# Performance work log

Hardware: AMD Instinct MI355X
Metric: run time of the kernel (lower is better)

The kernel has to match this reference:

```python
import jax, jax.numpy as jnp
import numpy as np

EMB, HEADS, T_BLK = 1024, 16, 2048
B, T = 2, 2048
HD = EMB // HEADS


def setup_inputs() -> dict:
    key = jax.random.key(0)
    ks = jax.random.split(key, 9)
    s = 1.0 / np.sqrt(EMB)
    return {
        "x": jax.random.normal(ks[0], (B, T, EMB), jnp.float32),
        "Wq": jax.random.normal(ks[1], (EMB, EMB), jnp.float32) * s,
        "bq": jax.random.normal(ks[2], (EMB,), jnp.float32) * s,
        "Wk": jax.random.normal(ks[3], (EMB, EMB), jnp.float32) * s,
        "bk": jax.random.normal(ks[4], (EMB,), jnp.float32) * s,
        "Wv": jax.random.normal(ks[5], (EMB, EMB), jnp.float32) * s,
        "bv": jax.random.normal(ks[6], (EMB,), jnp.float32) * s,
        "Wo": jax.random.normal(ks[7], (EMB, EMB), jnp.float32) * s,
        "bo": jax.random.normal(ks[8], (EMB,), jnp.float32) * s,
    }


def reference(x, Wq, bq, Wk, bk, Wv, bv, Wo, bo):
    # eval mode: dropout is identity
    Bn, Tn, C = x.shape
    def proj(W, b):
        y = x @ W.T + b                      # [B,T,C]
        return y.reshape(Bn, Tn, HEADS, HD).transpose(0, 2, 1, 3)  # [B,H,T,hd]
    q, k, v = proj(Wq, bq), proj(Wk, bk), proj(Wv, bv)
    scores = jnp.einsum('bhqd,bhkd->bhqk', q, k) * (HD ** -0.5)  # [B,H,T,T]
    causal = jnp.tril(jnp.ones((Tn, Tn), dtype=bool))
    scores = jnp.where(causal, scores, -jnp.inf)
    w = jax.nn.softmax(scores, axis=-1)
    out = jnp.einsum('bhqk,bhkd->bhqd', w, v)                    # [B,H,T,hd]
    out = out.transpose(0, 2, 1, 3).reshape(Bn, Tn, C)
    return out @ Wo.T + bo
```

## Files before the change

kernel.cpp:

```cpp
#include <hip/hip_runtime.h>
#include <stdint.h>

#define EMB   1024
#define HEADS 16
#define HD    64
#define BB    2
#define TT    2048
#define MTOT  (BB*TT)

#define ELX (4194304u)
#define ELW (1048576u)

#define CSCALE (0.125f * 1.44269504088896f)

typedef __attribute__((ext_vector_type(8))) short short8;
typedef __attribute__((ext_vector_type(4))) float f32x4;
typedef __attribute__((ext_vector_type(4))) unsigned short us4;

__device__ __forceinline__ float bf2f(ushort u) {
  union { uint32_t u; float f; } x; x.u = ((uint32_t)u) << 16; return x.f;
}
__device__ __forceinline__ ushort f2bf(float f) {
  union { float f; uint32_t u; } x; x.f = f;
  uint32_t u = x.u;
  u += 0x7fffu + ((u >> 16) & 1u);
  return (ushort)(u >> 16);
}
__device__ __forceinline__ uint32_t pack2(uint32_t lo, uint32_t hi) {
  return (lo >> 16) | (hi & 0xFFFF0000u);
}
__device__ __forceinline__ short8 pack8(f32x4 a, f32x4 b) {
  union { f32x4 v; uint32_t u[4]; } A, B;
  A.v = a; B.v = b;
  union { uint32_t d[4]; short8 s; } R;
  R.d[0] = pack2(A.u[0], A.u[1]);
  R.d[1] = pack2(A.u[2], A.u[3]);
  R.d[2] = pack2(B.u[0], B.u[1]);
  R.d[3] = pack2(B.u[2], B.u[3]);
  return R.s;
}
__device__ __forceinline__ short8 cvt8_rne(const float* f) {
  f32x4 a = *(const f32x4*)f;
  f32x4 b = *(const f32x4*)(f + 4);
  short8 r;
  r[0] = (short)f2bf(a[0]); r[1] = (short)f2bf(a[1]);
  r[2] = (short)f2bf(a[2]); r[3] = (short)f2bf(a[3]);
  r[4] = (short)f2bf(b[0]); r[5] = (short)f2bf(b[1]);
  r[6] = (short)f2bf(b[2]); r[7] = (short)f2bf(b[3]);
  return r;
}

__device__ __forceinline__ void gll16(const void* g, void* l) {
  __builtin_amdgcn_global_load_lds((const __attribute__((address_space(1))) void*)g,
                                   (__attribute__((address_space(3))) void*)l,
                                   16, 0, 0);
}

__device__ __forceinline__ int probe_dtype(const uint32_t* __restrict__ x) {
  const int lane = threadIdx.x & 63;
  int cnt = 0;
#pragma unroll
  for (int i = 0; i < 4; ++i) {
    const uint32_t v = x[lane * 4 + i];
    const uint32_t e = ((v & 0xFFFFu) >> 7) & 0xFFu;
    cnt += (e >= 0x70u && e <= 0x8Fu) ? 1 : 0;
  }
#pragma unroll
  for (int off = 1; off < 64; off <<= 1) cnt += __shfl_xor(cnt, off);
  return (cnt > 128) ? 1 : 0;
}

__global__ __launch_bounds__(256) void convert4(const void* __restrict__ w0,
                                                const void* __restrict__ w1,
                                                const void* __restrict__ w2,
                                                const void* __restrict__ x,
                                                ushort* __restrict__ w3,
                                                ushort* __restrict__ xb,
                                                int* __restrict__ flag) {
  const int isbf = probe_dtype((const uint32_t*)x);
  if (blockIdx.x == 0 && threadIdx.x == 0) *flag = isbf;
  const size_t i = ((size_t)blockIdx.x * 256 + threadIdx.x) * 8;
  if (i < 3u * ELW) {
    const int wi = (int)(i >> 20);
    const size_t off = i & (ELW - 1);
    const void* src = (wi == 0) ? w0 : (wi == 1) ? w1 : w2;
    if (isbf) *(short8*)(w3 + i) = *(const short8*)((const ushort*)src + off);
    else      *(short8*)(w3 + i) = cvt8_rne((const float*)src + off);
  } else {
    const size_t j = i - 3u * ELW;
    if (isbf) *(short8*)(xb + j) = *(const short8*)((const ushort*)x + j);
    else      *(short8*)(xb + j) = cvt8_rne((const float*)x + j);
  }
}

#define ASZ (256 * 64)
#define BSZ (192 * 64)

__device__ __forceinline__ void qkv_core(const ushort* __restrict__ xb,
                                         const ushort* __restrict__ W,
                                         int m0, int n0r,
                                         ushort* As0, ushort* Bs0,
                                         f32x4 acc[8][3]) {
  const int tid  = threadIdx.x;
  const int w    = tid >> 6;
  const int lane = tid & 63;
  const int quad = lane >> 4;
  const int l16  = lane & 15;
  const int wr   = w >> 2, wc = w & 3;

  const int prow = tid >> 3;
  const int c    = tid & 7;
  const int sw   = c ^ (prow & 7);
  const int rsw  = l16 & 7;

  auto stageB = [&](ushort* dst, int kt) {
#pragma unroll
    for (int g = 0; g < 3; ++g)
      gll16(W + (size_t)(n0r + g * 64 + prow) * EMB + kt * 64 + sw * 8,
            dst + g * 4096 + w * 512);
  };
  auto stageA = [&](ushort* dst, int kt) {
#pragma unroll
    for (int g = 0; g < 4; ++g)
      gll16(xb + (size_t)(m0 + g * 64 + prow) * EMB + kt * 64 + sw * 8,
            dst + g * 4096 + w * 512);
  };
  auto compute = [&](const ushort* Ab, const ushort* Bb) {
    short8 bf_[3][2];
#pragma unroll
    for (int ni = 0; ni < 3; ++ni)
#pragma unroll
      for (int ks = 0; ks < 2; ++ks)
        bf_[ni][ks] = *(const short8*)&Bb[(wc * 48 + ni * 16 + l16) * 64 +
                                          ((ks * 4 + quad) ^ rsw) * 8];
#pragma unroll
    for (int mi = 0; mi < 8; ++mi) {
      const int arow = (wr * 128 + mi * 16 + l16) * 64;
      short8 a0 = *(const short8*)&Ab[arow + ((quad) ^ rsw) * 8];
      short8 a1 = *(const short8*)&Ab[arow + ((4 + quad) ^ rsw) * 8];
#pragma unroll
      for (int ni = 0; ni < 3; ++ni) {
        acc[mi][ni] = __builtin_amdgcn_mfma_f32_16x16x32_bf16(a0, bf_[ni][0], acc[mi][ni], 0, 0, 0);
        acc[mi][ni] = __builtin_amdgcn_mfma_f32_16x16x32_bf16(a1, bf_[ni][1], acc[mi][ni], 0, 0, 0);
      }
    }
  };

  stageB(Bs0, 0);
  stageA(As0, 0);
  __syncthreads();

  for (int tp = 0; tp < 8; ++tp) {
    const int t0 = 2 * tp;
    stageB(Bs0 + BSZ, t0 + 1);
    stageA(As0 + ASZ, t0 + 1);
    compute(As0, Bs0);
    __syncthreads();
    if (tp < 7) {
      stageB(Bs0, t0 + 2);
      stageA(As0, t0 + 2);
    }
    compute(As0 + ASZ, Bs0 + BSZ);
    __syncthreads();
  }
}

__global__ __launch_bounds__(512, 2) void qkv_pipe(const ushort* __restrict__ xb,
                                                   const ushort* __restrict__ w3,
                                                   const void* __restrict__ bq,
                                                   const void* __restrict__ bk,
                                                   const void* __restrict__ bv,
                                                   ushort* __restrict__ qo,
                                                   ushort* __restrict__ ko,
                                                   ushort* __restrict__ vo,
                                                   const int* __restrict__ flag) {
  __shared__ __align__(16) ushort As2[2 * ASZ];
  __shared__ __align__(16) ushort Bs2[2 * BSZ];
  const int bid = blockIdx.x;
  const int xcd = bid & 7;
  const int mt  = xcd * 2 + ((bid >> 3) & 1);
  const int nt  = bid >> 4;
  const int m0  = mt * 256;
  const int n0r = nt * 192;

  f32x4 acc[8][3];
#pragma unroll
  for (int a = 0; a < 8; ++a)
#pragma unroll
    for (int b = 0; b < 3; ++b) acc[a][b] = (f32x4){0.f, 0.f, 0.f, 0.f};

  qkv_core(xb, w3, m0, n0r, As2, Bs2, acc);

  const int isbf = *flag;
  const int tid  = threadIdx.x;
  const int w    = tid >> 6;
  const int lane = tid & 63;
  const int quad = lane >> 4;
  const int l16  = lane & 15;
  const int wr   = w >> 2, wc = w & 3;

#pragma unroll
  for (int ni = 0; ni < 3; ++ni) {
    const int n   = n0r + wc * 48 + ni * 16 + l16;
    const int mat = n >> 10, nn = n & 1023;
    const void* bias = (mat == 0) ? bq : (mat == 1) ? bk : bv;
    const float bv_ = isbf ? bf2f(((const ushort*)bias)[nn]) : ((const float*)bias)[nn];
    const int h = nn >> 6, d = nn & 63;
    const float sc = (mat == 0) ? CSCALE : 1.0f;
    ushort* dqk = (mat == 0) ? qo : ko;
#pragma unroll
    for (int mi = 0; mi < 8; ++mi) {
      const int m = m0 + wr * 128 + mi * 16 + quad * 4;
      const int b = m >> 11, tt = m & (TT - 1);
      if (mat == 2) {
        us4 pk;
#pragma unroll
        for (int r = 0; r < 4; ++r) pk[r] = f2bf(acc[mi][ni][r] + bv_);
        *(us4*)&vo[((size_t)((b * HEADS + h) * HD + d)) * TT + tt] = pk;
      } else {
#pragma unroll
        for (int r = 0; r < 4; ++r)
          dqk[((size_t)((b * HEADS + h) * TT + tt + r)) * HD + d] =
              f2bf((acc[mi][ni][r] + bv_) * sc);
      }
    }
  }
}

__global__ __launch_bounds__(256) void attn3(const ushort* __restrict__ qw,
                                             const ushort* __restrict__ kw,
                                             const ushort* __restrict__ vtw,
                                             ushort* __restrict__ out) {
  __shared__ __align__(16) ushort Ks[2][64 * 64];
  __shared__ __align__(16) ushort Vts[2][64 * 64];
  __shared__ __align__(16) ushort Ps[4][16 * 64];

  const int bid = blockIdx.x;
  const int j  = bid >> 8;
  const int r8 = bid & 255;
  const int qh = r8 & 31;
  const int bh = j * 8 + (r8 >> 5);
  int qt;
  if      (j == 0) qt = qh;
  else if (j == 1) qt = 31 - qh;
  else if (j == 2) qt = (qh + 16) & 31;
  else             qt = 31 - ((qh + 16) & 31);
  const int h = bh & (HEADS - 1);
  const int b = bh >> 4;

  const int tid  = threadIdx.x;
  const int w    = tid >> 6;
  const int lane = tid & 63;
  const int quad = lane >> 4;
  const int l16  = lane & 15;
  const int rsw  = l16 & 7;

  const size_t hoff = ((size_t)(b * HEADS + h)) * TT * HD;
  const ushort* Qg = qw + hoff;
  const ushort* Kg = kw + hoff;
  const ushort* Vg = vtw + hoff;
  const int q0 = qt * 64;

  short8 qf[2];
  {
    const ushort* qrow = Qg + (size_t)(q0 + w * 16 + l16) * HD;
    qf[0] = *(const short8*)(qrow + quad * 8);
    qf[1] = *(const short8*)(qrow + 32 + quad * 8);
  }

  const int row = tid >> 2;
  const int cq  = (tid & 3) * 2;
  const int s0  = (cq)     ^ (row & 7);
  const int s1  = (cq + 1) ^ (row & 7);
  const int c0  = cq * 8;
  const ushort* Kbase = Kg + (size_t)row * HD + c0;
  const ushort* Vbase = Vg + (size_t)row * TT + c0;

  float lsp[4] = {0.f, 0.f, 0.f, 0.f};
  f32x4 O[4];
#pragma unroll
  for (int ni = 0; ni < 4; ++ni) O[ni] = (f32x4){0.f, 0.f, 0.f, 0.f};

  auto loadT = [&](int kt, short8& k0, short8& k1, short8& v0, short8& v1) {
    const size_t ko_ = (size_t)kt * 64 * HD;
    k0 = *(const short8*)(Kbase + ko_);
    k1 = *(const short8*)(Kbase + ko_ + 8);
    v0 = *(const short8*)(Vbase + kt * 64);
    v1 = *(const short8*)(Vbase + kt * 64 + 8);
  };
  auto writeT = [&](int buf, short8 k0, short8 k1, short8 v0, short8 v1) {
    *(short8*)&Ks[buf][row * 64 + s0 * 8]  = k0;
    *(short8*)&Ks[buf][row * 64 + s1 * 8]  = k1;
    *(short8*)&Vts[buf][row * 64 + s0 * 8] = v0;
    *(short8*)&Vts[buf][row * 64 + s1 * 8] = v1;
  };

  auto compute_tile = [&](int kt, int buf) {
    f32x4 s[4];
#pragma unroll
    for (int ni = 0; ni < 4; ++ni) s[ni] = (f32x4){0.f, 0.f, 0.f, 0.f};
#pragma unroll
    for (int ks = 0; ks < 2; ++ks) {
#pragma unroll
      for (int ni = 0; ni < 4; ++ni) {
        short8 kb = *(const short8*)&Ks[buf][(ni * 16 + l16) * 64 +
                                            ((ks * 4 + quad) ^ rsw) * 8];
        s[ni] = __builtin_amdgcn_mfma_f32_16x16x32_bf16(kb, qf[ks], s[ni], 0, 0, 0);
      }
    }
    if (kt == qt) {
      const int qq = w * 16 + l16;
#pragma unroll
      for (int ni = 0; ni < 4; ++ni) {
#pragma unroll
        for (int r = 0; r < 4; ++r)
          if (ni * 16 + quad * 4 + r > qq) s[ni][r] = -__builtin_inff();
      }
    }
#pragma unroll
    for (int ni = 0; ni < 4; ++ni) {
      union { float f; uint32_t u; } p0, p1, p2, p3;
      p0.f = exp2f(s[ni][0]); p1.f = exp2f(s[ni][1]);
      p2.f = exp2f(s[ni][2]); p3.f = exp2f(s[ni][3]);
      lsp[ni] += (p0.f + p1.f) + (p2.f + p3.f);
      uint2 dw;
      dw.x = pack2(p0.u, p1.u);
      dw.y = pack2(p2.u, p3.u);
      const int slot = (2 * ni + (quad >> 1)) ^ rsw;
      *(uint2*)&Ps[w][l16 * 64 + slot * 8 + (quad & 1) * 4] = dw;
    }
#pragma unroll
    for (int ks = 0; ks < 2; ++ks) {
      short8 a = *(const short8*)&Ps[w][l16 * 64 + ((ks * 4 + quad) ^ rsw) * 8];
#pragma unroll
      for (int ni = 0; ni < 4; ++ni) {
        short8 vb = *(const short8*)&Vts[buf][(ni * 16 + l16) * 64 +
                                              ((ks * 4 + quad) ^ rsw) * 8];
        O[ni] = __builtin_amdgcn_mfma_f32_16x16x32_bf16(a, vb, O[ni], 0, 0, 0);
      }
    }
  };

  short8 ek0, ek1, ev0, ev1;
  short8 ok0, ok1, ov0, ov1;
  loadT(0, ek0, ek1, ev0, ev1);
  if (qt >= 1) loadT(1, ok0, ok1, ov0, ov1);

  for (int pt = 0; ; ++pt) {
    const int t0 = 2 * pt, t1 = t0 + 1;
    __syncthreads();
    writeT(0, ek0, ek1, ev0, ev1);
    if (t1 <= qt) writeT(1, ok0, ok1, ov0, ov1);
    if (t0 + 2 <= qt) loadT(t0 + 2, ek0, ek1, ev0, ev1);
    if (t1 + 2 <= qt) loadT(t1 + 2, ok0, ok1, ov0, ov1);
    __syncthreads();
    compute_tile(t0, 0);
    if (t1 <= qt) compute_tile(t1, 1);
    if (t1 >= qt) break;
  }

  float lst = (lsp[0] + lsp[1]) + (lsp[2] + lsp[3]);
  lst += __shfl_xor(lst, 16);
  lst += __shfl_xor(lst, 32);

#pragma unroll
  for (int r = 0; r < 4; ++r) {
    const float inv = 1.0f / __shfl(lst, (lane & 48) | (quad * 4 + r));
    const int t = q0 + w * 16 + quad * 4 + r;
#pragma unroll
    for (int ni = 0; ni < 4; ++ni) {
      out[((size_t)(b * TT + t)) * EMB + h * HD + ni * 16 + l16] = f2bf(O[ni][r] * inv);
    }
  }
}

#define PASZ (128 * 64)

template<bool WBF>
__device__ __forceinline__ void proj_core(const ushort* __restrict__ A,
                                          const void* __restrict__ Wo,
                                          int m0, int n0,
                                          ushort* As2, ushort* Bs2,
                                          f32x4 acc[4][2]) {
  const int tid  = threadIdx.x;
  const int w    = tid >> 6;
  const int lane = tid & 63;
  const int quad = lane >> 4;
  const int l16  = lane & 15;
  const int wr   = w >> 2, wc = w & 3;

  const int prow = tid >> 3;
  const int sw   = (tid & 7) ^ (prow & 7);
  const int rsw  = l16 & 7;

  const ushort* Wu = (const ushort*)Wo;
  const float*  Wf = (const float*)Wo;
  f32x4 wreg[4];

  auto stageA = [&](ushort* dst, int kt) {
#pragma unroll
    for (int g = 0; g < 2; ++g)
      gll16(A + (size_t)(m0 + g * 64 + prow) * EMB + kt * 64 + sw * 8,
            dst + g * 4096 + w * 512);
  };
  auto stageB_gll = [&](ushort* dst, int kt) {
#pragma unroll
    for (int g = 0; g < 2; ++g)
      gll16(Wu + (size_t)(n0 + g * 64 + prow) * EMB + kt * 64 + sw * 8,
            dst + g * 4096 + w * 512);
  };
  auto stageB_issue = [&](int kt) {
#pragma unroll
    for (int g = 0; g < 2; ++g) {
      const float* src = Wf + (size_t)(n0 + g * 64 + prow) * EMB + kt * 64 + sw * 8;
      wreg[2 * g]     = *(const f32x4*)(src);
      wreg[2 * g + 1] = *(const f32x4*)(src + 4);
    }
  };
  auto stageB_write = [&](ushort* dst) {
#pragma unroll
    for (int g = 0; g < 2; ++g)
      *(short8*)&dst[((size_t)g * 512 + tid) * 8] = pack8(wreg[2 * g], wreg[2 * g + 1]);
  };
  auto compute = [&](const ushort* Ab, const ushort* Bb) {
    short8 bf_[2][2];
#pragma unroll
    for (int ni = 0; ni < 2; ++ni)
#pragma unroll
      for (int ks = 0; ks < 2; ++ks)
        bf_[ni][ks] = *(const short8*)&Bb[(wc * 32 + ni * 16 + l16) * 64 +
                                          ((ks * 4 + quad) ^ rsw) * 8];
#pragma unroll
    for (int mi = 0; mi < 4; ++mi) {
      const int arow = (wr * 64 + mi * 16 + l16) * 64;
      short8 a0 = *(const short8*)&Ab[arow + ((quad) ^ rsw) * 8];
      short8 a1 = *(const short8*)&Ab[arow + ((4 + quad) ^ rsw) * 8];
#pragma unroll
      for (int ni = 0; ni < 2; ++ni) {
        acc[mi][ni] = __builtin_amdgcn_mfma_f32_16x16x32_bf16(a0, bf_[ni][0], acc[mi][ni], 0, 0, 0);
        acc[mi][ni] = __builtin_amdgcn_mfma_f32_16x16x32_bf16(a1, bf_[ni][1], acc[mi][ni], 0, 0, 0);
      }
    }
  };

  stageA(As2, 0);
  if constexpr (WBF) stageB_gll(Bs2, 0);
  else { stageB_issue(0); stageB_write(Bs2); }
  __syncthreads();

  for (int tp = 0; tp < 8; ++tp) {
    const int t0 = 2 * tp;
    stageA(As2 + PASZ, t0 + 1);
    if constexpr (WBF) stageB_gll(Bs2 + PASZ, t0 + 1);
    else stageB_issue(t0 + 1);
    compute(As2, Bs2);
    if constexpr (!WBF) stageB_write(Bs2 + PASZ);
    __syncthreads();
    if (tp < 7) {
      stageA(As2, t0 + 2);
      if constexpr (WBF) stageB_gll(Bs2, t0 + 2);
      else stageB_issue(t0 + 2);
    }
    compute(As2 + PASZ, Bs2 + PASZ);
    if constexpr (!WBF) { if (tp < 7) stageB_write(Bs2); }
    __syncthreads();
  }
}

__global__ __launch_bounds__(512, 2) void proj_pipe(const ushort* __restrict__ A,
                                                    const void* __restrict__ Wo,
                                                    const void* __restrict__ bo,
                                                    void* __restrict__ out,
                                                    const int* __restrict__ flag) {
  __shared__ __align__(16) ushort As2[2 * PASZ];
  __shared__ __align__(16) ushort Bs2[2 * PASZ];
  const int bid = blockIdx.x;
  const int xcd = bid & 7;
  const int mt  = xcd * 4 + ((bid >> 3) & 3);
  const int nt  = bid >> 5;
  const int m0  = mt * 128;
  const int n0  = nt * 128;

  f32x4 acc[4][2];
#pragma unroll
  for (int i = 0; i < 4; ++i)
#pragma unroll
    for (int jj = 0; jj < 2; ++jj) acc[i][jj] = (f32x4){0.f, 0.f, 0.f, 0.f};

  const int isbf = *flag;
  if (isbf) proj_core<true >(A, Wo, m0, n0, As2, Bs2, acc);
  else      proj_core<false>(A, Wo, m0, n0, As2, Bs2, acc);

  const int tid  = threadIdx.x;
  const int w    = tid >> 6;
  const int lane = tid & 63;
  const int quad = lane >> 4;
  const int l16  = lane & 15;
  const int wr   = w >> 2, wc = w & 3;

#pragma unroll
  for (int ni = 0; ni < 2; ++ni) {
    const int n = n0 + wc * 32 + ni * 16 + l16;
    const float bv_ = isbf ? bf2f(((const ushort*)bo)[n]) : ((const float*)bo)[n];
#pragma unroll
    for (int mi = 0; mi < 4; ++mi) {
#pragma unroll
      for (int r = 0; r < 4; ++r) {
        const int m = m0 + wr * 64 + mi * 16 + quad * 4 + r;
        const float v = acc[mi][ni][r] + bv_;
        if (isbf) ((ushort*)out)[(size_t)m * EMB + n] = f2bf(v);
        else      ((float*) out)[(size_t)m * EMB + n] = v;
      }
    }
  }
}

extern "C" void kernel_launch(void* const* d_in, const int* in_sizes, int n_in,
                              void* d_out, int out_size, void* d_ws, size_t ws_size,
                              hipStream_t stream) {
  const void* x  = d_in[0];
  const void* Wq = d_in[1];
  const void* bq = d_in[2];
  const void* Wk = d_in[3];
  const void* bk = d_in[4];
  const void* Wv = d_in[5];
  const void* bv = d_in[6];
  const void* Wo = d_in[7];
  const void* bo = d_in[8];

  int* flag = (int*)d_ws;
  ushort* base = (ushort*)((char*)d_ws + 256);

  ushort* q_ws  = base;
  ushort* k_ws  = q_ws + ELX;
  ushort* vt_ws = k_ws + ELX;
  ushort* w3    = vt_ws + ELX;
  ushort* o_ws  = vt_ws + ELX;
  ushort* xb    = (ushort*)d_out;

  convert4<<<dim3(3584), dim3(256), 0, stream>>>(Wq, Wk, Wv, x, w3, xb, flag);
  qkv_pipe<<<dim3(256), dim3(512), 0, stream>>>(xb, w3, bq, bk, bv,
                                                q_ws, k_ws, vt_ws, flag);
  attn3<<<dim3(1024), dim3(256), 0, stream>>>(q_ws, k_ws, vt_ws, o_ws);
  proj_pipe<<<dim3(256), dim3(512), 0, stream>>>(o_ws, Wo, bo, d_out, flag);
}
```

Baseline: 199.5 us.

## Retile QKV GEMM to 128x128 single-buffered tiles with more blocks

Replaces the 256x192 double-buffered QKV projection tile (512 threads, 256 blocks) with a 128x128 single-buffered tile on 256 threads and 768 blocks. Each block now covers a single Q/K/V matrix, so the bias pointer and scale are chosen once per block. The aim is better occupancy and load balance across the CUs with less LDS per block. The cost is lower data reuse per tile and no overlap of global loads with MFMA work, since there is now a sync before and after every k-step.

```diff
diff --git a/kernel.cpp b/kernel.cpp
--- a/kernel.cpp
+++ b/kernel.cpp
@@ -93,79 +93,56 @@
   }
 }
 
-#define ASZ (256 * 64)
-#define BSZ (192 * 64)
+#define QSZ (128 * 64)
 
 __device__ __forceinline__ void qkv_core(const ushort* __restrict__ xb,
                                          const ushort* __restrict__ W,
                                          int m0, int n0r,
-                                         ushort* As0, ushort* Bs0,
-                                         f32x4 acc[8][3]) {
+                                         ushort* As, ushort* Bs,
+                                         f32x4 acc[4][4]) {
   const int tid  = threadIdx.x;
   const int w    = tid >> 6;
   const int lane = tid & 63;
   const int quad = lane >> 4;
   const int l16  = lane & 15;
-  const int wr   = w >> 2, wc = w & 3;
+  const int wr   = w >> 1, wc = w & 1;
 
   const int prow = tid >> 3;
-  const int c    = tid & 7;
-  const int sw   = c ^ (prow & 7);
+  const int sw   = (tid & 7) ^ (prow & 7);
   const int rsw  = l16 & 7;
 
-  auto stageB = [&](ushort* dst, int kt) {
-#pragma unroll
-    for (int g = 0; g < 3; ++g)
-      gll16(W + (size_t)(n0r + g * 64 + prow) * EMB + kt * 64 + sw * 8,
-            dst + g * 4096 + w * 512);
-  };
-  auto stageA = [&](ushort* dst, int kt) {
+  for (int kt = 0; kt < 16; ++kt) {
+    __syncthreads();
 #pragma unroll
     for (int g = 0; g < 4; ++g)
-      gll16(xb + (size_t)(m0 + g * 64 + prow) * EMB + kt * 64 + sw * 8,
-            dst + g * 4096 + w * 512);
-  };
-  auto compute = [&](const ushort* Ab, const ushort* Bb) {
-    short8 bf_[3][2];
-#pragma unroll
-    for (int ni = 0; ni < 3; ++ni)
-#pragma unroll
-      for (int ks = 0; ks < 2; ++ks)
-        bf_[ni][ks] = *(const short8*)&Bb[(wc * 48 + ni * 16 + l16) * 64 +
-                                          ((ks * 4 + quad) ^ rsw) * 8];
-#pragma unroll
-    for (int mi = 0; mi < 8; ++mi) {
-      const int arow = (wr * 128 + mi * 16 + l16) * 64;
-      short8 a0 = *(const short8*)&Ab[arow + ((quad) ^ rsw) * 8];
-      short8 a1 = *(const short8*)&Ab[arow + ((4 + quad) ^ rsw) * 8];
-#pragma unroll
-      for (int ni = 0; ni < 3; ++ni) {
-        acc[mi][ni] = __builtin_amdgcn_mfma_f32_16x16x32_bf16(a0, bf_[ni][0], acc[mi][ni], 0, 0, 0);
-        acc[mi][ni] = __builtin_amdgcn_mfma_f32_16x16x32_bf16(a1, bf_[ni][1], acc[mi][ni], 0, 0, 0);
-      }
-    }
-  };
-
-  stageB(Bs0, 0);
-  stageA(As0, 0);
-  __syncthreads();
-
-  for (int tp = 0; tp < 8; ++tp) {
-    const int t0 = 2 * tp;
-    stageB(Bs0 + BSZ, t0 + 1);
-    stageA(As0 + ASZ, t0 + 1);
-    compute(As0, Bs0);
+      gll16(xb + (size_t)(m0 + g * 32 + prow) * EMB + kt * 64 + sw * 8,
+            As + g * 2048 + w * 512);
+#pragma unroll
+    for (int g = 0; g < 4; ++g)
+      gll16(W + (size_t)(n0r + g * 32 + prow) * EMB + kt * 64 + sw * 8,
+            Bs + g * 2048 + w * 512);
     __syncthreads();
-    if (tp < 7) {
-      stageB(Bs0, t0 + 2);
-      stageA(As0, t0 + 2);
-    }
-    compute(As0 + ASZ, Bs0 + BSZ);
-    __syncthreads();
-  }
-}
-
-__global__ __launch_bounds__(512, 2) void qkv_pipe(const ushort* __restrict__ xb,
+
+#pragma unroll
+    for (int ks = 0; ks < 2; ++ks) {
+      const int pc = (ks * 4 + quad) ^ rsw;
+      short8 a_[4], b_[4];
+#pragma unroll
+      for (int mi = 0; mi < 4; ++mi)
+        a_[mi] = *(const short8*)&As[(wr * 64 + mi * 16 + l16) * 64 + pc * 8];
+#pragma unroll
+      for (int ni = 0; ni < 4; ++ni)
+        b_[ni] = *(const short8*)&Bs[(wc * 64 + ni * 16 + l16) * 64 + pc * 8];
+#pragma unroll
+      for (int mi = 0; mi < 4; ++mi)
+#pragma unroll
+        for (int ni = 0; ni < 4; ++ni)
+          acc[mi][ni] = __builtin_amdgcn_mfma_f32_16x16x32_bf16(a_[mi], b_[ni], acc[mi][ni], 0, 0, 0);
+    }
+  }
+}
+
+__global__ __launch_bounds__(256, 3) void qkv_pipe(const ushort* __restrict__ xb,
                                                    const ushort* __restrict__ w3,
                                                    const void* __restrict__ bq,
                                                    const void* __restrict__ bk,
@@ -174,22 +151,25 @@
                                                    ushort* __restrict__ ko,
                                                    ushort* __restrict__ vo,
                                                    const int* __restrict__ flag) {
-  __shared__ __align__(16) ushort As2[2 * ASZ];
-  __shared__ __align__(16) ushort Bs2[2 * BSZ];
+  __shared__ __align__(16) ushort As[QSZ];
+  __shared__ __align__(16) ushort Bs[QSZ];
   const int bid = blockIdx.x;
   const int xcd = bid & 7;
-  const int mt  = xcd * 2 + ((bid >> 3) & 1);
-  const int nt  = bid >> 4;
-  const int m0  = mt * 256;
-  const int n0r = nt * 192;
-
-  f32x4 acc[8][3];
-#pragma unroll
-  for (int a = 0; a < 8; ++a)
-#pragma unroll
-    for (int b = 0; b < 3; ++b) acc[a][b] = (f32x4){0.f, 0.f, 0.f, 0.f};
-
-  qkv_core(xb, w3, m0, n0r, As2, Bs2, acc);
+  const int mt  = xcd * 4 + ((bid >> 3) & 3);
+  const int nt  = bid >> 5;
+  const int m0  = mt * 128;
+  const int mat = nt >> 3;
+  const int n0r = (nt & 7) * 128;
+  const ushort* Wp = w3 + (size_t)mat * ELW;
+  const void* bias = (mat == 0) ? bq : (mat == 1) ? bk : bv;
+
+  f32x4 acc[4][4];
+#pragma unroll
+  for (int a = 0; a < 4; ++a)
+#pragma unroll
+    for (int b = 0; b < 4; ++b) acc[a][b] = (f32x4){0.f, 0.f, 0.f, 0.f};
+
+  qkv_core(xb, Wp, m0, n0r, As, Bs, acc);
 
   const int isbf = *flag;
   const int tid  = threadIdx.x;
@@ -197,20 +177,18 @@
   const int lane = tid & 63;
   const int quad = lane >> 4;
   const int l16  = lane & 15;
-  const int wr   = w >> 2, wc = w & 3;
-
-#pragma unroll
-  for (int ni = 0; ni < 3; ++ni) {
-    const int n   = n0r + wc * 48 + ni * 16 + l16;
-    const int mat = n >> 10, nn = n & 1023;
-    const void* bias = (mat == 0) ? bq : (mat == 1) ? bk : bv;
-    const float bv_ = isbf ? bf2f(((const ushort*)bias)[nn]) : ((const float*)bias)[nn];
-    const int h = nn >> 6, d = nn & 63;
-    const float sc = (mat == 0) ? CSCALE : 1.0f;
-    ushort* dqk = (mat == 0) ? qo : ko;
-#pragma unroll
-    for (int mi = 0; mi < 8; ++mi) {
-      const int m = m0 + wr * 128 + mi * 16 + quad * 4;
+  const int wr   = w >> 1, wc = w & 1;
+  ushort* dqk = (mat == 0) ? qo : ko;
+  const float sc = (mat == 0) ? CSCALE : 1.0f;
+
+#pragma unroll
+  for (int ni = 0; ni < 4; ++ni) {
+    const int n = n0r + wc * 64 + ni * 16 + l16;
+    const float bv_ = isbf ? bf2f(((const ushort*)bias)[n]) : ((const float*)bias)[n];
+    const int h = n >> 6, d = n & 63;
+#pragma unroll
+    for (int mi = 0; mi < 4; ++mi) {
+      const int m = m0 + wr * 64 + mi * 16 + quad * 4;
       const int b = m >> 11, tt = m & (TT - 1);
       if (mat == 2) {
         us4 pk;
@@ -539,7 +517,7 @@
   ushort* xb    = (ushort*)d_out;
 
   convert4<<<dim3(3584), dim3(256), 0, stream>>>(Wq, Wk, Wv, x, w3, xb, flag);
-  qkv_pipe<<<dim3(256), dim3(512), 0, stream>>>(xb, w3, bq, bk, bv,
+  qkv_pipe<<<dim3(768), dim3(256), 0, stream>>>(xb, w3, bq, bk, bv,
                                                 q_ws, k_ws, vt_ws, flag);
   attn3<<<dim3(1024), dim3(256), 0, stream>>>(q_ws, k_ws, vt_ws, o_ws);
   proj_pipe<<<dim3(256), dim3(512), 0, stream>>>(o_ws, Wo, bo, d_out, flag);
```

New measurement: 195.5 us. 1.02x faster.
